# Kernel optimization log

Measured on AMD Instinct MI355X. Metric: run time of the kernel, lower is better.

The kernel has to match this reference:

```python
import jax, jax.numpy as jnp
import numpy as np

D_MODEL = 1024
N_HEADS = 16
D_HEAD = D_MODEL // N_HEADS
D_FF = 4096
EPS = 1e-5
NEG = -1e10


def setup_inputs() -> dict:
    key = jax.random.key(0)
    ks = jax.random.split(key, 16)
    s = 0.02
    x = jax.random.normal(ks[0], (4, 1024, D_MODEL), dtype=jnp.float32)
    mask = jnp.ones((4, 1, 1, 1024), dtype=jnp.int32)
    return {
        "x": x,
        "mask": mask,
        "Wq": jax.random.normal(ks[1], (D_MODEL, D_MODEL), jnp.float32) * s,
        "Wk": jax.random.normal(ks[2], (D_MODEL, D_MODEL), jnp.float32) * s,
        "Wv": jax.random.normal(ks[3], (D_MODEL, D_MODEL), jnp.float32) * s,
        "Wp": jax.random.normal(ks[4], (D_MODEL, D_MODEL), jnp.float32) * s,
        "bp": jnp.zeros((D_MODEL,), jnp.float32),
        "W1": jax.random.normal(ks[5], (D_MODEL, D_FF), jnp.float32) * s,
        "b1": jnp.zeros((D_FF,), jnp.float32),
        "W2": jax.random.normal(ks[6], (D_FF, D_MODEL), jnp.float32) * s,
        "b2": jnp.zeros((D_MODEL,), jnp.float32),
        "g1": jnp.ones((D_MODEL,), jnp.float32),
        "be1": jnp.zeros((D_MODEL,), jnp.float32),
        "g2": jnp.ones((D_MODEL,), jnp.float32),
        "be2": jnp.zeros((D_MODEL,), jnp.float32),
    }


def _layer_norm(x, g, b):
    mu = jnp.mean(x, axis=-1, keepdims=True)
    var = jnp.mean(jnp.square(x - mu), axis=-1, keepdims=True)
    return (x - mu) * jax.lax.rsqrt(var + EPS) * g + b


def _mha(x, mask, Wq, Wk, Wv, Wp, bp):
    B, L, _ = x.shape
    q = (x @ Wq).reshape(B, L, N_HEADS, D_HEAD).transpose(0, 2, 1, 3)  # (B,H,L,dh)
    k = (x @ Wk).reshape(B, L, N_HEADS, D_HEAD).transpose(0, 2, 1, 3)
    v = (x @ Wv).reshape(B, L, N_HEADS, D_HEAD).transpose(0, 2, 1, 3)
    scores = jnp.einsum('bhqd,bhkd->bhqk', q, k) / jnp.sqrt(jnp.float32(D_HEAD))
    scores = jnp.where(mask == 0, NEG, scores)
    attn = jax.nn.softmax(scores, axis=-1)
    heads = jnp.einsum('bhqk,bhkd->bhqd', attn, v)  # (B,H,L,dh)
    heads = heads.transpose(0, 2, 1, 3).reshape(B, L, D_MODEL)
    return heads @ Wp + bp


def reference(x, mask, Wq, Wk, Wv, Wp, bp, W1, b1, W2, b2, g1, be1, g2, be2):
    # Post-norm residual sublayers (dropout inactive at inference)
    attn_out = _mha(x, mask, Wq, Wk, Wv, Wp, bp)
    h = _layer_norm(x + attn_out, g1, be1)
    ff = jax.nn.relu(h @ W1 + b1) @ W2 + b2
    out = _layer_norm(h + ff, g2, be2)
    return out
```

## Files before the change

### kernel.cpp

```cpp
#include <hip/hip_runtime.h>
#include <hip/hip_bf16.h>

typedef __attribute__((ext_vector_type(8))) short short8;
typedef __attribute__((ext_vector_type(4))) short short4v;
typedef __attribute__((ext_vector_type(4))) float float4v;

static __device__ __forceinline__ float b2f(short s) {
    return __builtin_bit_cast(float, ((unsigned)(unsigned short)s) << 16);
}
static __device__ __forceinline__ short f2b(float f) {
    unsigned x = __builtin_bit_cast(unsigned, f);
    unsigned r = (x + 0x7fffu + ((x >> 16) & 1u)) >> 16;
    return (short)r;
}
static __device__ __forceinline__ void gload_lds16(const short* g, short* l) {
    __builtin_amdgcn_global_load_lds(
        (const __attribute__((address_space(1))) void*)g,
        (__attribute__((address_space(3))) void*)l, 16, 0, 0);
}

static __device__ __forceinline__ void tile_transpose(const float* __restrict__ in,
                                                      short* __restrict__ out,
                                                      int R, int C, int bx, int by,
                                                      float tile[64][65])
{
    const int tx = threadIdx.x;
    const int r0 = by * 64, c0 = bx * 64;
    const int lr = tx >> 4, lc = (tx & 15) * 4;
#pragma unroll
    for (int p = 0; p < 4; p++) {
        const float4v v = *(const float4v*)&in[(size_t)(r0 + lr + p * 16) * C + c0 + lc];
#pragma unroll
        for (int j = 0; j < 4; j++) tile[lr + p * 16][lc + j] = v[j];
    }
    __syncthreads();
    const int oc = tx >> 3, orr = (tx & 7) * 8;
#pragma unroll
    for (int p = 0; p < 2; p++) {
        const int c = oc + p * 32;
        short8 pk;
#pragma unroll
        for (int j = 0; j < 8; j++) pk[j] = f2b(tile[orr + j][c]);
        *(short8*)&out[(size_t)(c0 + c) * R + r0 + orr] = pk;
    }
}

__global__ __launch_bounds__(256) void prep_k(const float* __restrict__ x,
                                              const float* __restrict__ Wq,
                                              const float* __restrict__ Wk,
                                              const float* __restrict__ Wv,
                                              const float* __restrict__ Wp,
                                              const float* __restrict__ W1,
                                              const float* __restrict__ W2,
                                              short* __restrict__ xb,
                                              short* __restrict__ WqkvT,
                                              short* __restrict__ WpT,
                                              short* __restrict__ W1T,
                                              short* __restrict__ W2T)
{
    __shared__ float tile[64][65];
    const int b = blockIdx.x;
    if (b < 4096) {
        const size_t i = ((size_t)b * 256 + threadIdx.x) * 4;
        const float4v v = *(const float4v*)&x[i];
        short4v s;
#pragma unroll
        for (int j = 0; j < 4; j++) s[j] = f2b(v[j]);
        *(short4v*)&xb[i] = s;
    } else if (b < 5120) {
        const int lb = b - 4096;
        const int wsel = lb >> 8, t = lb & 255;
        const float* in = (wsel == 0) ? Wq : (wsel == 1) ? Wk : (wsel == 2) ? Wv : Wp;
        short* out = (wsel < 3) ? (WqkvT + ((size_t)wsel << 20)) : WpT;
        tile_transpose(in, out, 1024, 1024, t & 15, t >> 4, tile);
    } else if (b < 6144) {
        const int lb = b - 5120;
        tile_transpose(W1, W1T, 1024, 4096, lb & 63, lb >> 6, tile);
    } else {
        const int lb = b - 6144;
        tile_transpose(W2, W2T, 4096, 1024, lb & 15, lb >> 4, tile);
    }
}

template<int MODE, int BM, int BN, int KH, int WM_, int WN_>
__global__ __launch_bounds__(256) void gemm_bt(const short* __restrict__ X,
                                               const short* __restrict__ Wt,
                                               short* __restrict__ out,
                                               const float* __restrict__ bias,
                                               const short* __restrict__ res,
                                               int M, int N, int K)
{
    constexpr int MI = WM_ / 16, NI = WN_ / 16;
    constexpr int NWX = BN / WN_;
    __shared__ short As[KH][BM * 32];
    __shared__ short Bs[KH][BN * 32];
    const int tid = threadIdx.x;
    const int wave = tid >> 6, lane = tid & 63;
    const int quad = lane >> 4, l16 = lane & 15;

    int bx = blockIdx.x, by = blockIdx.y;
    {
        const int nbx = gridDim.x, nby = gridDim.y;
        if ((nby & 7) == 0) {
            const int g = by * nbx + bx;
            const int xcd = g & 7, local = g >> 3, Y = nby >> 3;
            by = xcd * Y + (local % Y);
            bx = local / Y;
        }
    }
    const int m0 = by * BM, n0 = bx * BN;
    const int wm = (wave / NWX) * WM_, wn = (wave % NWX) * WN_;

    int kb = 0, ke = K;
    short* op = out;
    if (MODE == 5) {
        kb = blockIdx.z * (K >> 1);
        ke = kb + (K >> 1);
        op = out + (size_t)blockIdx.z * M * N;
    }

    const int srow = tid >> 2, sc8 = (tid & 3) * 8;

    float4v acc[MI][NI] = {};

    for (int k0 = kb; k0 < ke; k0 += KH * 32) {
#pragma unroll
        for (int c = 0; c < BM / 64; c++)
#pragma unroll
            for (int h = 0; h < KH; h++)
                gload_lds16(X + (size_t)(m0 + c * 64 + srow) * K + k0 + h * 32 + sc8,
                            &As[h][(c * 256 + tid) * 8]);
#pragma unroll
        for (int c = 0; c < BN / 64; c++)
#pragma unroll
            for (int h = 0; h < KH; h++)
                gload_lds16(Wt + (size_t)(n0 + c * 64 + srow) * K + k0 + h * 32 + sc8,
                            &Bs[h][(c * 256 + tid) * 8]);
        __syncthreads();
#pragma unroll
        for (int h = 0; h < KH; h++) {
            short8 af[MI], bf[NI];
#pragma unroll
            for (int i = 0; i < MI; i++) af[i] = *(const short8*)&As[h][(wm + i * 16 + l16) * 32 + quad * 8];
#pragma unroll
            for (int i = 0; i < NI; i++) bf[i] = *(const short8*)&Bs[h][(wn + i * 16 + l16) * 32 + quad * 8];
#pragma unroll
            for (int mi = 0; mi < MI; mi++)
#pragma unroll
                for (int ni = 0; ni < NI; ni++)
                    acc[mi][ni] = __builtin_amdgcn_mfma_f32_16x16x32_bf16(af[mi], bf[ni], acc[mi][ni], 0, 0, 0);
        }
        __syncthreads();
    }

#pragma unroll
    for (int mi = 0; mi < MI; mi++) {
#pragma unroll
        for (int ni = 0; ni < NI; ni++) {
            const int gn = n0 + wn + ni * 16 + l16;
            const float bv = (MODE == 2) ? bias[gn] : 0.0f;
            if (MODE == 4 && (gn >> 10) == 2) {
                const int gmb = m0 + wm + mi * 16 + quad * 4;
                const int d = gn & 63;
                const size_t a = ((size_t)2 << 22) + ((size_t)((gmb >> 10) * 16 + ((gn & 1023) >> 6)) << 16)
                               + ((size_t)d << 10) + (gmb & 1023);
                short4v w;
#pragma unroll
                for (int r = 0; r < 4; r++) w[r] = f2b(acc[mi][ni][r]);
                *(short4v*)&out[a] = w;
                continue;
            }
#pragma unroll
            for (int r = 0; r < 4; r++) {
                const int gm = m0 + wm + mi * 16 + quad * 4 + r;
                float v = acc[mi][ni][r];
                if (MODE == 4) {
                    const int s = gn >> 10;
                    const int n = gn & 1023;
                    const int hh = n >> 6, d = n & 63;
                    const size_t bh16 = (size_t)((gm >> 10) * 16 + hh) << 16;
                    const size_t base = (size_t)s << 22;
                    if (s == 0) out[base + bh16 + ((size_t)(gm & 1023) << 6) + d] = f2b(v * 0.125f);
                    else        out[base + bh16 + ((size_t)(gm & 1023) << 6) + d] = f2b(v);
                } else if (MODE == 2) {
                    v += bv;
                    v = fmaxf(v, 0.0f);
                    out[(size_t)gm * N + gn] = f2b(v);
                } else {
                    op[(size_t)gm * N + gn] = f2b(v);
                }
            }
        }
    }
}

__global__ __launch_bounds__(256) void attn_k(const short* __restrict__ Qb,
                                              const short* __restrict__ Kb,
                                              const short* __restrict__ Vt,
                                              const int* __restrict__ mask,
                                              short* __restrict__ heads)
{
    __shared__ short Kl[2][64 * 32];
    __shared__ short Vl[2][64 * 32];
    __shared__ short P[4][16 * 72];
    const int bh = blockIdx.x, qb = blockIdx.y;
    const int b = bh >> 4, h = bh & 15;
    const int tid = threadIdx.x, wave = tid >> 6, lane = tid & 63;
    const int quad = lane >> 4, l16 = lane & 15;
    const int qbase = qb * 64 + wave * 16;
    const short* Qp = Qb + ((size_t)bh << 16) + (size_t)qbase * 64;
    const short* Kp = Kb + ((size_t)bh << 16);
    const short* Vp = Vt + ((size_t)bh << 16);
    const int* mp = mask + (b << 10);

    const short8 bq0 = *(const short8*)&Qp[l16 * 64 + quad * 8];
    const short8 bq1 = *(const short8*)&Qp[l16 * 64 + 32 + quad * 8];

    float rs = 0.0f;
    float4v o[4] = {};
    short* myP = &P[wave][0];

    const int srow = tid >> 2, sc8 = (tid & 3) * 8;

    for (int kc = 0; kc < 1024; kc += 64) {
        gload_lds16(Kp + (size_t)(kc + srow) * 64 + sc8,      &Kl[0][tid * 8]);
        gload_lds16(Kp + (size_t)(kc + srow) * 64 + 32 + sc8, &Kl[1][tid * 8]);
        gload_lds16(Vp + (size_t)srow * 1024 + kc + sc8,      &Vl[0][tid * 8]);
        gload_lds16(Vp + (size_t)srow * 1024 + kc + 32 + sc8, &Vl[1][tid * 8]);
        __syncthreads();

        float4v s[4];
#pragma unroll
        for (int kt = 0; kt < 4; kt++) {
            s[kt] = (float4v){};
            const short8 ka = *(const short8*)&Kl[0][(kt * 16 + l16) * 32 + quad * 8];
            s[kt] = __builtin_amdgcn_mfma_f32_16x16x32_bf16(ka, bq0, s[kt], 0, 0, 0);
            const short8 kb = *(const short8*)&Kl[1][(kt * 16 + l16) * 32 + quad * 8];
            s[kt] = __builtin_amdgcn_mfma_f32_16x16x32_bf16(kb, bq1, s[kt], 0, 0, 0);
        }
#pragma unroll
        for (int kt = 0; kt < 4; kt++) {
            const int4 mv = *(const int4*)&mp[kc + kt * 16 + quad * 4];
            float p0 = mv.x ? __expf(fminf(s[kt][0], 30.f)) : 0.f;
            float p1 = mv.y ? __expf(fminf(s[kt][1], 30.f)) : 0.f;
            float p2 = mv.z ? __expf(fminf(s[kt][2], 30.f)) : 0.f;
            float p3 = mv.w ? __expf(fminf(s[kt][3], 30.f)) : 0.f;
            rs += (p0 + p1) + (p2 + p3);
            short4v w;
            w[0] = f2b(p0); w[1] = f2b(p1); w[2] = f2b(p2); w[3] = f2b(p3);
            *(short4v*)&myP[l16 * 72 + kt * 16 + quad * 4] = w;
        }
        const short8 bp0 = *(const short8*)&myP[l16 * 72 + quad * 8];
        const short8 bp1 = *(const short8*)&myP[l16 * 72 + 32 + quad * 8];
#pragma unroll
        for (int dt = 0; dt < 4; dt++) {
            const short8 va = *(const short8*)&Vl[0][(dt * 16 + l16) * 32 + quad * 8];
            o[dt] = __builtin_amdgcn_mfma_f32_16x16x32_bf16(va, bp0, o[dt], 0, 0, 0);
            const short8 vb = *(const short8*)&Vl[1][(dt * 16 + l16) * 32 + quad * 8];
            o[dt] = __builtin_amdgcn_mfma_f32_16x16x32_bf16(vb, bp1, o[dt], 0, 0, 0);
        }
        __syncthreads();
    }

    rs += __shfl_xor(rs, 16);
    rs += __shfl_xor(rs, 32);
    const float inv = 1.0f / fmaxf(rs, 1e-20f);
    const int gq = qbase + l16;
#pragma unroll
    for (int dt = 0; dt < 4; dt++) {
        short4v w;
#pragma unroll
        for (int r = 0; r < 4; r++) w[r] = f2b(o[dt][r] * inv);
        *(short4v*)&heads[((size_t)(b * 1024 + gq) << 10) + h * 64 + dt * 16 + quad * 4] = w;
    }
}

template<bool F32OUT>
__global__ __launch_bounds__(256) void red_ln_k(const short* __restrict__ p0,
                                                const short* __restrict__ p1,
                                                const float* __restrict__ bias,
                                                const short* __restrict__ res,
                                                const float* __restrict__ g,
                                                const float* __restrict__ be,
                                                short* __restrict__ outb,
                                                float* __restrict__ outf)
{
    __shared__ float red[8];
    const int row = blockIdx.x, tid = threadIdx.x;
    const size_t base = ((size_t)row << 10) + tid * 4;
    const short4v a = *(const short4v*)&p0[base];
    const short4v b = *(const short4v*)&p1[base];
    const short4v c = *(const short4v*)&res[base];
    const float4v bv = *(const float4v*)&bias[tid * 4];
    float v[4];
#pragma unroll
    for (int i = 0; i < 4; i++) v[i] = b2f(a[i]) + b2f(b[i]) + bv[i] + b2f(c[i]);
    float s = v[0] + v[1] + v[2] + v[3];
#pragma unroll
    for (int off = 32; off; off >>= 1) s += __shfl_xor(s, off);
    if ((tid & 63) == 0) red[tid >> 6] = s;
    __syncthreads();
    const float mu = (red[0] + red[1] + red[2] + red[3]) * (1.0f / 1024.0f);
    float vs = 0.f;
#pragma unroll
    for (int i = 0; i < 4; i++) { const float d = v[i] - mu; vs += d * d; }
#pragma unroll
    for (int off = 32; off; off >>= 1) vs += __shfl_xor(vs, off);
    if ((tid & 63) == 0) red[4 + (tid >> 6)] = vs;
    __syncthreads();
    const float rstd = rsqrtf((red[4] + red[5] + red[6] + red[7]) * (1.0f / 1024.0f) + 1e-5f);
    const float4v gv = *(const float4v*)&g[tid * 4];
    const float4v bev = *(const float4v*)&be[tid * 4];
    if (F32OUT) {
        float4v w;
#pragma unroll
        for (int i = 0; i < 4; i++) w[i] = (v[i] - mu) * rstd * gv[i] + bev[i];
        *(float4v*)&outf[base] = w;
    } else {
        short4v w;
#pragma unroll
        for (int i = 0; i < 4; i++) w[i] = f2b((v[i] - mu) * rstd * gv[i] + bev[i]);
        *(short4v*)&outb[base] = w;
    }
}

extern "C" void kernel_launch(void* const* d_in, const int* in_sizes, int n_in,
                              void* d_out, int out_size, void* d_ws, size_t ws_size,
                              hipStream_t stream)
{
    const float* x   = (const float*)d_in[0];
    const int*   mk  = (const int*)d_in[1];
    const float* Wq  = (const float*)d_in[2];
    const float* Wk  = (const float*)d_in[3];
    const float* Wv  = (const float*)d_in[4];
    const float* Wp  = (const float*)d_in[5];
    const float* bp  = (const float*)d_in[6];
    const float* W1  = (const float*)d_in[7];
    const float* b1  = (const float*)d_in[8];
    const float* W2  = (const float*)d_in[9];
    const float* b2  = (const float*)d_in[10];
    const float* g1  = (const float*)d_in[11];
    const float* be1 = (const float*)d_in[12];
    const float* g2  = (const float*)d_in[13];
    const float* be2 = (const float*)d_in[14];
    float* out = (float*)d_out;

    char* ws = (char*)d_ws;
    const size_t MB = (size_t)1 << 20;
    short* xb     = (short*)(ws + 0 * MB);
    short* WqkvT  = (short*)(ws + 8 * MB);
    short* WpT    = (short*)(ws + 14 * MB);
    short* W1T    = (short*)(ws + 16 * MB);
    short* W2T    = (short*)(ws + 24 * MB);
    short* Qb     = (short*)(ws + 32 * MB);
    short* Kb     = (short*)(ws + 40 * MB);
    short* Vt     = (short*)(ws + 48 * MB);
    short* hd     = (short*)(ws + 56 * MB);
    short* partP  = (short*)(ws + 32 * MB);
    short* u      = (short*)(ws + 32 * MB);
    short* partF  = (short*)(ws + 0 * MB);
    short* hbuf   = (short*)(ws + 72 * MB);

    const dim3 blk(256);

    prep_k<<<dim3(7168), blk, 0, stream>>>(x, Wq, Wk, Wv, Wp, W1, W2,
                                           xb, WqkvT, WpT, W1T, W2T);

    gemm_bt<4, 128, 128, 2, 64, 64><<<dim3(24, 32), blk, 0, stream>>>(xb, WqkvT, Qb, nullptr, nullptr, 4096, 3072, 1024);

    attn_k<<<dim3(64, 16), blk, 0, stream>>>(Qb, Kb, Vt, mk, hd);

    gemm_bt<5, 128, 128, 2, 64, 64><<<dim3(8, 32, 2), blk, 0, stream>>>(hd, WpT, partP, nullptr, nullptr, 4096, 1024, 1024);

    red_ln_k<false><<<dim3(4096), blk, 0, stream>>>(partP, partP + (4u << 20), bp, xb, g1, be1, hbuf, nullptr);

    gemm_bt<2, 128, 256, 2, 64, 128><<<dim3(16, 32), blk, 0, stream>>>(hbuf, W1T, u, b1, nullptr, 4096, 4096, 1024);

    gemm_bt<5, 128, 128, 2, 64, 64><<<dim3(8, 32, 2), blk, 0, stream>>>(u, W2T, partF, nullptr, nullptr, 4096, 1024, 4096);

    red_ln_k<true><<<dim3(4096), blk, 0, stream>>>(partF, partF + (4u << 20), b2, hbuf, g2, be2, nullptr, out);
}
```

Measured before the change: 359.8 us.

## Split FFN2 GEMM K four ways, use 128x128 FFN1 tiles, widen attention K/V chunks

The W2 GEMM now splits K across four z-slices instead of two, writing the extra partials to spare workspace regions passed through the bias/res pointers, and the final reduce-LN sums four partials. The W1 GEMM switches from 128x256 tiles to 128x128, which doubles its grid, and the GEMM template drops its warp-tile parameters. The attention kernel loads 128 keys per iteration and processes them in two 64-key passes, halving the number of block barriers. The intent is more parallelism for the K-heavy GEMM and fewer synchronisations in attention, at the cost of more partial-sum traffic and more attention LDS.

Measured after the change: 362.6 us. Within noise of the previous version (+0.8%).

```diff
diff --git a/kernel.cpp b/kernel.cpp
--- a/kernel.cpp
+++ b/kernel.cpp
@@ -82,7 +82,7 @@
     }
 }
 
-template<int MODE, int BM, int BN, int KH, int WM_, int WN_>
+template<int MODE, int BM, int BN, int KH>
 __global__ __launch_bounds__(256) void gemm_bt(const short* __restrict__ X,
                                                const short* __restrict__ Wt,
                                                short* __restrict__ out,
@@ -90,8 +90,7 @@
                                                const short* __restrict__ res,
                                                int M, int N, int K)
 {
-    constexpr int MI = WM_ / 16, NI = WN_ / 16;
-    constexpr int NWX = BN / WN_;
+    constexpr int MI = BM / 32, NI = BN / 32;
     __shared__ short As[KH][BM * 32];
     __shared__ short Bs[KH][BN * 32];
     const int tid = threadIdx.x;
@@ -109,14 +108,19 @@
         }
     }
     const int m0 = by * BM, n0 = bx * BN;
-    const int wm = (wave / NWX) * WM_, wn = (wave % NWX) * WN_;
+    const int wm = (wave >> 1) * 64, wn = (wave & 1) * 64;
 
     int kb = 0, ke = K;
     short* op = out;
     if (MODE == 5) {
-        kb = blockIdx.z * (K >> 1);
-        ke = kb + (K >> 1);
-        op = out + (size_t)blockIdx.z * M * N;
+        const int kq = K / gridDim.z;
+        kb = blockIdx.z * kq;
+        ke = kb + kq;
+        const size_t MN = (size_t)M * N;
+        op = (blockIdx.z == 0) ? out
+           : (blockIdx.z == 1) ? out + MN
+           : (blockIdx.z == 2) ? (short*)bias
+           :                     (short*)res;
     }
 
     const int srow = tid >> 2, sc8 = (tid & 3) * 8;
@@ -200,8 +204,8 @@
                                               const int* __restrict__ mask,
                                               short* __restrict__ heads)
 {
-    __shared__ short Kl[2][64 * 32];
-    __shared__ short Vl[2][64 * 32];
+    __shared__ short Kl[2][128 * 32];
+    __shared__ short Vl[4][64 * 32];
     __shared__ short P[4][16 * 72];
     const int bh = blockIdx.x, qb = blockIdx.y;
     const int b = bh >> 4, h = bh & 15;
@@ -222,42 +226,50 @@
 
     const int srow = tid >> 2, sc8 = (tid & 3) * 8;
 
-    for (int kc = 0; kc < 1024; kc += 64) {
-        gload_lds16(Kp + (size_t)(kc + srow) * 64 + sc8,      &Kl[0][tid * 8]);
-        gload_lds16(Kp + (size_t)(kc + srow) * 64 + 32 + sc8, &Kl[1][tid * 8]);
-        gload_lds16(Vp + (size_t)srow * 1024 + kc + sc8,      &Vl[0][tid * 8]);
-        gload_lds16(Vp + (size_t)srow * 1024 + kc + 32 + sc8, &Vl[1][tid * 8]);
+    for (int kc = 0; kc < 1024; kc += 128) {
+        gload_lds16(Kp + (size_t)(kc + srow) * 64 + sc8,           &Kl[0][tid * 8]);
+        gload_lds16(Kp + (size_t)(kc + srow) * 64 + 32 + sc8,      &Kl[1][tid * 8]);
+        gload_lds16(Kp + (size_t)(kc + 64 + srow) * 64 + sc8,      &Kl[0][(256 + tid) * 8]);
+        gload_lds16(Kp + (size_t)(kc + 64 + srow) * 64 + 32 + sc8, &Kl[1][(256 + tid) * 8]);
+        gload_lds16(Vp + (size_t)srow * 1024 + kc + sc8,           &Vl[0][tid * 8]);
+        gload_lds16(Vp + (size_t)srow * 1024 + kc + 32 + sc8,      &Vl[1][tid * 8]);
+        gload_lds16(Vp + (size_t)srow * 1024 + kc + 64 + sc8,      &Vl[2][tid * 8]);
+        gload_lds16(Vp + (size_t)srow * 1024 + kc + 96 + sc8,      &Vl[3][tid * 8]);
         __syncthreads();
 
-        float4v s[4];
-#pragma unroll
-        for (int kt = 0; kt < 4; kt++) {
-            s[kt] = (float4v){};
-            const short8 ka = *(const short8*)&Kl[0][(kt * 16 + l16) * 32 + quad * 8];
-            s[kt] = __builtin_amdgcn_mfma_f32_16x16x32_bf16(ka, bq0, s[kt], 0, 0, 0);
-            const short8 kb = *(const short8*)&Kl[1][(kt * 16 + l16) * 32 + quad * 8];
-            s[kt] = __builtin_amdgcn_mfma_f32_16x16x32_bf16(kb, bq1, s[kt], 0, 0, 0);
-        }
-#pragma unroll
-        for (int kt = 0; kt < 4; kt++) {
-            const int4 mv = *(const int4*)&mp[kc + kt * 16 + quad * 4];
-            float p0 = mv.x ? __expf(fminf(s[kt][0], 30.f)) : 0.f;
-            float p1 = mv.y ? __expf(fminf(s[kt][1], 30.f)) : 0.f;
-            float p2 = mv.z ? __expf(fminf(s[kt][2], 30.f)) : 0.f;
-            float p3 = mv.w ? __expf(fminf(s[kt][3], 30.f)) : 0.f;
-            rs += (p0 + p1) + (p2 + p3);
-            short4v w;
-            w[0] = f2b(p0); w[1] = f2b(p1); w[2] = f2b(p2); w[3] = f2b(p3);
-            *(short4v*)&myP[l16 * 72 + kt * 16 + quad * 4] = w;
-        }
-        const short8 bp0 = *(const short8*)&myP[l16 * 72 + quad * 8];
-        const short8 bp1 = *(const short8*)&myP[l16 * 72 + 32 + quad * 8];
-#pragma unroll
-        for (int dt = 0; dt < 4; dt++) {
-            const short8 va = *(const short8*)&Vl[0][(dt * 16 + l16) * 32 + quad * 8];
-            o[dt] = __builtin_amdgcn_mfma_f32_16x16x32_bf16(va, bp0, o[dt], 0, 0, 0);
-            const short8 vb = *(const short8*)&Vl[1][(dt * 16 + l16) * 32 + quad * 8];
-            o[dt] = __builtin_amdgcn_mfma_f32_16x16x32_bf16(vb, bp1, o[dt], 0, 0, 0);
+#pragma unroll
+        for (int pass = 0; pass < 2; pass++) {
+            const int P64 = pass * 64;
+            float4v s[4];
+#pragma unroll
+            for (int kt = 0; kt < 4; kt++) {
+                s[kt] = (float4v){};
+                const short8 ka = *(const short8*)&Kl[0][(P64 + kt * 16 + l16) * 32 + quad * 8];
+                s[kt] = __builtin_amdgcn_mfma_f32_16x16x32_bf16(ka, bq0, s[kt], 0, 0, 0);
+                const short8 kb = *(const short8*)&Kl[1][(P64 + kt * 16 + l16) * 32 + quad * 8];
+                s[kt] = __builtin_amdgcn_mfma_f32_16x16x32_bf16(kb, bq1, s[kt], 0, 0, 0);
+            }
+#pragma unroll
+            for (int kt = 0; kt < 4; kt++) {
+                const int4 mv = *(const int4*)&mp[kc + P64 + kt * 16 + quad * 4];
+                float p0 = mv.x ? __expf(fminf(s[kt][0], 30.f)) : 0.f;
+                float p1 = mv.y ? __expf(fminf(s[kt][1], 30.f)) : 0.f;
+                float p2 = mv.z ? __expf(fminf(s[kt][2], 30.f)) : 0.f;
+                float p3 = mv.w ? __expf(fminf(s[kt][3], 30.f)) : 0.f;
+                rs += (p0 + p1) + (p2 + p3);
+                short4v w;
+                w[0] = f2b(p0); w[1] = f2b(p1); w[2] = f2b(p2); w[3] = f2b(p3);
+                *(short4v*)&myP[l16 * 72 + kt * 16 + quad * 4] = w;
+            }
+            const short8 bp0 = *(const short8*)&myP[l16 * 72 + quad * 8];
+            const short8 bp1 = *(const short8*)&myP[l16 * 72 + 32 + quad * 8];
+#pragma unroll
+            for (int dt = 0; dt < 4; dt++) {
+                const short8 va = *(const short8*)&Vl[2 * pass][(dt * 16 + l16) * 32 + quad * 8];
+                o[dt] = __builtin_amdgcn_mfma_f32_16x16x32_bf16(va, bp0, o[dt], 0, 0, 0);
+                const short8 vb = *(const short8*)&Vl[2 * pass + 1][(dt * 16 + l16) * 32 + quad * 8];
+                o[dt] = __builtin_amdgcn_mfma_f32_16x16x32_bf16(vb, bp1, o[dt], 0, 0, 0);
+            }
         }
         __syncthreads();
     }
@@ -275,9 +287,11 @@
     }
 }
 
-template<bool F32OUT>
+template<int NP, bool F32OUT>
 __global__ __launch_bounds__(256) void red_ln_k(const short* __restrict__ p0,
                                                 const short* __restrict__ p1,
+                                                const short* __restrict__ p2,
+                                                const short* __restrict__ p3,
                                                 const float* __restrict__ bias,
                                                 const short* __restrict__ res,
                                                 const float* __restrict__ g,
@@ -295,6 +309,12 @@
     float v[4];
 #pragma unroll
     for (int i = 0; i < 4; i++) v[i] = b2f(a[i]) + b2f(b[i]) + bv[i] + b2f(c[i]);
+    if (NP == 4) {
+        const short4v a2 = *(const short4v*)&p2[base];
+        const short4v a3 = *(const short4v*)&p3[base];
+#pragma unroll
+        for (int i = 0; i < 4; i++) v[i] += b2f(a2[i]) + b2f(a3[i]);
+    }
     float s = v[0] + v[1] + v[2] + v[3];
 #pragma unroll
     for (int off = 32; off; off >>= 1) s += __shfl_xor(s, off);
@@ -358,7 +378,9 @@
     short* hd     = (short*)(ws + 56 * MB);
     short* partP  = (short*)(ws + 32 * MB);
     short* u      = (short*)(ws + 32 * MB);
-    short* partF  = (short*)(ws + 0 * MB);
+    short* pF0    = (short*)(ws + 0 * MB);
+    short* pF2    = (short*)(ws + 16 * MB);
+    short* pF3    = (short*)(ws + 64 * MB);
     short* hbuf   = (short*)(ws + 72 * MB);
 
     const dim3 blk(256);
@@ -366,17 +388,19 @@
     prep_k<<<dim3(7168), blk, 0, stream>>>(x, Wq, Wk, Wv, Wp, W1, W2,
                                            xb, WqkvT, WpT, W1T, W2T);
 
-    gemm_bt<4, 128, 128, 2, 64, 64><<<dim3(24, 32), blk, 0, stream>>>(xb, WqkvT, Qb, nullptr, nullptr, 4096, 3072, 1024);
+    gemm_bt<4, 128, 128, 2><<<dim3(24, 32), blk, 0, stream>>>(xb, WqkvT, Qb, nullptr, nullptr, 4096, 3072, 1024);
 
     attn_k<<<dim3(64, 16), blk, 0, stream>>>(Qb, Kb, Vt, mk, hd);
 
-    gemm_bt<5, 128, 128, 2, 64, 64><<<dim3(8, 32, 2), blk, 0, stream>>>(hd, WpT, partP, nullptr, nullptr, 4096, 1024, 1024);
-
-    red_ln_k<false><<<dim3(4096), blk, 0, stream>>>(partP, partP + (4u << 20), bp, xb, g1, be1, hbuf, nullptr);
-
-    gemm_bt<2, 128, 256, 2, 64, 128><<<dim3(16, 32), blk, 0, stream>>>(hbuf, W1T, u, b1, nullptr, 4096, 4096, 1024);
-
-    gemm_bt<5, 128, 128, 2, 64, 64><<<dim3(8, 32, 2), blk, 0, stream>>>(u, W2T, partF, nullptr, nullptr, 4096, 1024, 4096);
-
-    red_ln_k<true><<<dim3(4096), blk, 0, stream>>>(partF, partF + (4u << 20), b2, hbuf, g2, be2, nullptr, out);
-}
+    gemm_bt<5, 128, 128, 2><<<dim3(8, 32, 2), blk, 0, stream>>>(hd, WpT, partP, nullptr, nullptr, 4096, 1024, 1024);
+
+    red_ln_k<2, false><<<dim3(4096), blk, 0, stream>>>(partP, partP + (4u << 20), partP, partP,
+                                                       bp, xb, g1, be1, hbuf, nullptr);
+
+    gemm_bt<2, 128, 128, 2><<<dim3(32, 32), blk, 0, stream>>>(hbuf, W1T, u, b1, nullptr, 4096, 4096, 1024);
+
+    gemm_bt<5, 128, 128, 2><<<dim3(8, 32, 4), blk, 0, stream>>>(u, W2T, pF0, (const float*)pF2, pF3, 4096, 1024, 4096);
+
+    red_ln_k<4, true><<<dim3(4096), blk, 0, stream>>>(pF0, pF0 + (4u << 20), pF2, pF3,
+                                                      b2, hbuf, g2, be2, nullptr, out);
+}
```
